# Optimization experiments

Hardware: AMD Instinct MI355X
Metric: run time of the kernel (lower is better)

Reference implementation:

```python
import jax, jax.numpy as jnp
import numpy as np

B, N, M, BUCKETS = 4096, 2048, 2048, 16
T = 100.0  # softmax temperature from module (self.T = 100)


def _make_values(buckets):
    b = buckets // 2
    v = np.zeros((buckets, 1), np.float32)
    for i in range(buckets):
        v[i, 0] = 1.0 / 2.0 ** (b - i) if i < b else -1.0 / 2.0 ** (i - b)
    return jnp.asarray(v)


def setup_inputs() -> dict:
    key = jax.random.key(0)
    ks = jax.random.split(key, 7)
    scale = 1.0 / np.sqrt(M)  # nn.Linear default init range
    return {
        "x": jax.random.normal(ks[0], (B, M), jnp.float32),
        "x_hash": jax.random.normal(ks[1], (B, M), jnp.float32),
        "weight": jax.random.uniform(ks[2], (N, M), jnp.float32, -scale, scale),
        "bias": jax.random.uniform(ks[3], (N,), jnp.float32, -scale, scale),
        "a0": jax.random.normal(ks[4], (BUCKETS, 1), jnp.float32),
        "a1": jax.random.normal(ks[5], (BUCKETS, 1), jnp.float32),
        "a2": jax.random.normal(ks[6], (BUCKETS, 1), jnp.float32),
        "values": _make_values(BUCKETS),
    }


def reference(x, x_hash, weight, bias, a0, a1, a2, values):
    n, m = weight.shape
    fcw = weight.reshape(1, -1)                       # [1, N*M]
    # rank-1 outer products + bias: fx [buckets, N*M]
    fx = a1 @ fcw + a2 @ (fcw * fcw) + a0
    probs = jax.nn.softmax(fx * T, axis=0)            # softmax over buckets
    hash_weight = (probs.T @ values).reshape(n, m)    # [N, M]
    out = x @ weight.T + bias                         # [B, N]
    out_hash = x_hash @ hash_weight.T + bias          # [B, N]
    return out, out_hash
```

## Files before the change

### kernel.cpp

```cpp
#include <hip/hip_runtime.h>
#include <hip/hip_bf16.h>

typedef __attribute__((ext_vector_type(8))) short bf16x8;
typedef __attribute__((ext_vector_type(4))) float f32x4;
typedef __attribute__((ext_vector_type(8))) unsigned short u16x8;
typedef __attribute__((ext_vector_type(4))) unsigned short u16x4;

__device__ __forceinline__ unsigned short f2bf_rtne(float f) {
    unsigned int u = __float_as_uint(f);
    u += 0x7FFFu + ((u >> 16) & 1u);
    return (unsigned short)(u >> 16);
}

__device__ __forceinline__ void gl2lds16(const void* g, void* l) {
    __builtin_amdgcn_global_load_lds((const __attribute__((address_space(1))) void*)g,
                                     (__attribute__((address_space(3))) void*)l, 16, 0, 0);
}

#define NB 16
__global__ void prep_all(const float* __restrict__ x, const float* __restrict__ xh,
                         const float* __restrict__ w,
                         const float* __restrict__ a0, const float* __restrict__ a1,
                         const float* __restrict__ a2, const float* __restrict__ vals,
                         unsigned short* __restrict__ xb, unsigned short* __restrict__ xhb,
                         unsigned short* __restrict__ wbf, unsigned short* __restrict__ hwbf) {
    const int job = blockIdx.y;
    const int stride = gridDim.x * blockDim.x;
    int i = blockIdx.x * blockDim.x + threadIdx.x;
    if (job < 2) {
        const float* in = job ? xh : x;
        unsigned short* out = job ? xhb : xb;
        const int n8 = (4096 * 2048) / 8;
        for (; i < n8; i += stride) {
            const float4* p = (const float4*)in + (size_t)i * 2;
            float4 v0 = p[0];
            float4 v1 = p[1];
            u16x8 r;
            r[0] = f2bf_rtne(v0.x); r[1] = f2bf_rtne(v0.y); r[2] = f2bf_rtne(v0.z); r[3] = f2bf_rtne(v0.w);
            r[4] = f2bf_rtne(v1.x); r[5] = f2bf_rtne(v1.y); r[6] = f2bf_rtne(v1.z); r[7] = f2bf_rtne(v1.w);
            *((u16x8*)out + i) = r;
        }
    } else {
        float A0[NB], A1[NB], A2[NB], V[NB];
#pragma unroll
        for (int b = 0; b < NB; ++b) {
            A0[b] = a0[b] * 100.0f;
            A1[b] = a1[b] * 100.0f;
            A2[b] = a2[b] * 100.0f;
            V[b]  = vals[b];
        }
        const int n4 = (2048 * 2048) / 4;
        for (; i < n4; i += stride) {
            float4 wv = ((const float4*)w)[i];
            float win[4] = {wv.x, wv.y, wv.z, wv.w};
            u16x4 wr, hr;
#pragma unroll
            for (int c = 0; c < 4; ++c) {
                float xx = win[c];
                float x2 = xx * xx;
                float l[NB];
                float mx = -1e30f;
#pragma unroll
                for (int b = 0; b < NB; ++b) {
                    l[b] = fmaf(A1[b], xx, fmaf(A2[b], x2, A0[b]));
                    mx = fmaxf(mx, l[b]);
                }
                float s = 0.0f, acc = 0.0f;
#pragma unroll
                for (int b = 0; b < NB; ++b) {
                    float e = __expf(l[b] - mx);
                    s += e;
                    acc = fmaf(e, V[b], acc);
                }
                wr[c] = f2bf_rtne(xx);
                hr[c] = f2bf_rtne(acc / s);
            }
            *((u16x4*)wbf + i)  = wr;
            *((u16x4*)hwbf + i) = hr;
        }
    }
}

__global__ __launch_bounds__(512, 2) void gemm256(
    const unsigned short* __restrict__ Ax, const unsigned short* __restrict__ Ah,
    const unsigned short* __restrict__ Bw, const unsigned short* __restrict__ Bh,
    const float* __restrict__ bias,
    float* __restrict__ Cx, float* __restrict__ Chh) {
    const int K = 2048, N = 2048;

    __shared__ unsigned short lds[65536];

    const unsigned short* A  = blockIdx.z ? Ah : Ax;
    const unsigned short* Bm = blockIdx.z ? Bh : Bw;
    float* C = blockIdx.z ? Chh : Cx;

    const int tid  = threadIdx.x;
    const int lane = tid & 63;
    const int wid  = tid >> 6;
    const int wr = wid >> 2;
    const int wc = wid & 3;
    const int fr = lane & 15;
    const int fq = lane >> 4;
    const int brow = blockIdx.x;
    const int bcol = blockIdx.y;

    const int srow = tid >> 3;
    const int sg8  = ((tid & 7) ^ (srow & 7)) * 8;
    const unsigned short* gA = A  + (size_t)(brow * 256 + srow) * K + sg8;
    const unsigned short* gB = Bm + (size_t)(bcol * 256 + srow) * K + sg8;
    const int wbase = wid * 512;

    const int g0 = (fq ^ (fr & 7)) * 8;
    const int g1 = g0 ^ 32;

#define STAGE_A(buf, h, j) {                                                    \
    const unsigned short* _g = gA + (size_t)((h) * 128) * K + (j) * 64;         \
    gl2lds16(_g,                  lds + (buf) * 16384 + (h) * 8192 + wbase);    \
    gl2lds16(_g + (size_t)64 * K, lds + (buf) * 16384 + (h) * 8192 + 4096 + wbase); }
#define STAGE_B(buf, h, j) {                                                    \
    const unsigned short* _g = gB + (size_t)((h) * 128) * K + (j) * 64;         \
    gl2lds16(_g,                  lds + 32768 + (buf) * 16384 + (h) * 8192 + wbase); \
    gl2lds16(_g + (size_t)64 * K, lds + 32768 + (buf) * 16384 + (h) * 8192 + 4096 + wbase); }

#define LDA(dst, buf, mblk) {                                                   \
    const unsigned short* _p = lds + (buf) * 16384 + (wr * 128 + (mblk) * 16 + fr) * 64; \
    dst[0] = *(const bf16x8*)(_p + g0);                                         \
    dst[1] = *(const bf16x8*)(_p + g1); }
#define LDB(dst, buf, nblk) {                                                   \
    const unsigned short* _p = lds + 32768 + (buf) * 16384 + (wc * 64 + (nblk) * 16 + fr) * 64; \
    dst[0] = *(const bf16x8*)(_p + g0);                                         \
    dst[1] = *(const bf16x8*)(_p + g1); }

#define MM(mi, n, kk, AF) acc[mi][n] = __builtin_amdgcn_mfma_f32_16x16x32_bf16(AF[kk], bfr[n][kk], acc[mi][n], 0, 0, 0)

#define PHASE(q, buf, STG, GATE) {                                              \
    if ((q) == 0) {                                                             \
        LDB(bfr[0], buf, 0); LDB(bfr[1], buf, 1);                               \
        LDB(bfr[2], buf, 2); LDB(bfr[3], buf, 3);                               \
    }                                                                           \
    LDA(af0, buf, 2 * (q)); LDA(af1, buf, 2 * (q) + 1);                         \
    STG;                                                                        \
    __builtin_amdgcn_s_barrier();                                               \
    asm volatile("s_waitcnt lgkmcnt(0)" ::: "memory");                          \
    __builtin_amdgcn_s_setprio(1);                                              \
    MM(2*(q),0,0,af0); MM(2*(q),0,1,af0); MM(2*(q)+1,0,0,af1); MM(2*(q)+1,0,1,af1); \
    MM(2*(q),1,0,af0); MM(2*(q),1,1,af0); MM(2*(q)+1,1,0,af1); MM(2*(q)+1,1,1,af1); \
    MM(2*(q),2,0,af0); MM(2*(q),2,1,af0); MM(2*(q)+1,2,0,af1); MM(2*(q)+1,2,1,af1); \
    MM(2*(q),3,0,af0); MM(2*(q),3,1,af0); MM(2*(q)+1,3,0,af1); MM(2*(q)+1,3,1,af1); \
    __builtin_amdgcn_s_setprio(0);                                              \
    GATE;                                                                       \
    __builtin_amdgcn_s_barrier(); }

    STAGE_A(0, 0, 0); STAGE_A(0, 1, 0);
    STAGE_B(0, 0, 0); STAGE_B(0, 1, 0);
    STAGE_B(1, 0, 1); STAGE_B(1, 1, 1);
    asm volatile("s_waitcnt vmcnt(4)" ::: "memory");
    __builtin_amdgcn_s_barrier();

    f32x4 acc[8][4] = {};
    bf16x8 bfr[4][2], af0[2], af1[2];

#pragma unroll 1
    for (int t = 0; t < 15; ++t) {
        const int j1 = 2 * t + 1, j2 = 2 * t + 2, j3 = 2 * t + 3;
        PHASE(0, 0, STAGE_A(1, 0, j1), );
        PHASE(1, 0, STAGE_A(1, 1, j1), );
        PHASE(2, 0, STAGE_B(0, 0, j2), );
        PHASE(3, 0, STAGE_B(0, 1, j2), asm volatile("s_waitcnt vmcnt(4)" ::: "memory"));
        PHASE(0, 1, STAGE_A(0, 0, j2), );
        PHASE(1, 1, STAGE_A(0, 1, j2), );
        PHASE(2, 1, STAGE_B(1, 0, j3), );
        PHASE(3, 1, STAGE_B(1, 1, j3), asm volatile("s_waitcnt vmcnt(4)" ::: "memory"));
    }
    PHASE(0, 0, STAGE_A(1, 0, 31), );
    PHASE(1, 0, STAGE_A(1, 1, 31), );
    PHASE(2, 0, , );
    PHASE(3, 0, , asm volatile("s_waitcnt vmcnt(0)" ::: "memory"));
    PHASE(0, 1, , );
    PHASE(1, 1, , );
    PHASE(2, 1, , );
    PHASE(3, 1, , );

#pragma unroll
    for (int n = 0; n < 4; ++n) {
        const int col = bcol * 256 + wc * 64 + n * 16 + fr;
        const float bv = bias[col];
#pragma unroll
        for (int m = 0; m < 8; ++m) {
            const int row0 = brow * 256 + wr * 128 + m * 16 + fq * 4;
#pragma unroll
            for (int r = 0; r < 4; ++r)
                C[(size_t)(row0 + r) * N + col] = acc[m][n][r] + bv;
        }
    }
#undef STAGE_A
#undef STAGE_B
#undef LDA
#undef LDB
#undef MM
#undef PHASE
}

extern "C" void kernel_launch(void* const* d_in, const int* in_sizes, int n_in,
                              void* d_out, int out_size, void* d_ws, size_t ws_size,
                              hipStream_t stream) {
    const float* x    = (const float*)d_in[0];
    const float* xh   = (const float*)d_in[1];
    const float* w    = (const float*)d_in[2];
    const float* bias = (const float*)d_in[3];
    const float* a0   = (const float*)d_in[4];
    const float* a1   = (const float*)d_in[5];
    const float* a2   = (const float*)d_in[6];
    const float* vals = (const float*)d_in[7];

    float* out  = (float*)d_out;
    float* outh = out + (size_t)4096 * 2048;

    char* ws = (char*)d_ws;
    unsigned short* xb  = (unsigned short*)(ws);
    unsigned short* xhb = (unsigned short*)(ws + (size_t)16 * 1024 * 1024);
    unsigned short* wb  = (unsigned short*)(ws + (size_t)32 * 1024 * 1024);
    unsigned short* hwb = (unsigned short*)(ws + (size_t)40 * 1024 * 1024);

    prep_all<<<dim3(1024, 3), 256, 0, stream>>>(x, xh, w, a0, a1, a2, vals, xb, xhb, wb, hwb);

    dim3 grid(4096 / 256, 2048 / 256, 2);
    gemm256<<<grid, 512, 0, stream>>>(xb, xhb, wb, hwb, bias, out, outh);
}
```

Baseline: 102.2 us.

## Switch GEMM inner loop to 32x32x16 bf16 MFMA tiles

Replaces the 16x16x32 MFMA tiling with 32x32x16 MFMA instructions. Each wave now computes a 4x2 grid of 32x32 accumulators, and the LDS fragment loads and the epilogue row mapping are reworked to match the new lane layout. Larger MFMA tiles raise arithmetic per LDS read and cut the instruction count per phase. The risk is a different LDS bank access pattern and longer MFMA dependency latency. The prep kernel grid is also doubled in x, which changes how that preprocessing work is split across blocks.

```diff
diff --git a/kernel.cpp b/kernel.cpp
--- a/kernel.cpp
+++ b/kernel.cpp
@@ -2,7 +2,7 @@
 #include <hip/hip_bf16.h>
 
 typedef __attribute__((ext_vector_type(8))) short bf16x8;
-typedef __attribute__((ext_vector_type(4))) float f32x4;
+typedef __attribute__((ext_vector_type(16))) float f32x16;
 typedef __attribute__((ext_vector_type(8))) unsigned short u16x8;
 typedef __attribute__((ext_vector_type(4))) unsigned short u16x4;
 
@@ -99,8 +99,8 @@
     const int wid  = tid >> 6;
     const int wr = wid >> 2;
     const int wc = wid & 3;
-    const int fr = lane & 15;
-    const int fq = lane >> 4;
+    const int l31 = lane & 31;
+    const int kh  = lane >> 5;
     const int brow = blockIdx.x;
     const int bcol = blockIdx.y;
 
@@ -110,8 +110,11 @@
     const unsigned short* gB = Bm + (size_t)(bcol * 256 + srow) * K + sg8;
     const int wbase = wid * 512;
 
-    const int g0 = (fq ^ (fr & 7)) * 8;
-    const int g1 = g0 ^ 32;
+    const int ax = lane & 7;
+    const int gq[4] = { ((0 + kh) ^ ax) * 8, ((2 + kh) ^ ax) * 8,
+                        ((4 + kh) ^ ax) * 8, ((6 + kh) ^ ax) * 8 };
+    const int aBase = (wr * 128 + l31) * 64;
+    const int bBase = 32768 + (wc * 64 + l31) * 64;
 
 #define STAGE_A(buf, h, j) {                                                    \
     const unsigned short* _g = gA + (size_t)((h) * 128) * K + (j) * 64;         \
@@ -122,31 +125,33 @@
     gl2lds16(_g,                  lds + 32768 + (buf) * 16384 + (h) * 8192 + wbase); \
     gl2lds16(_g + (size_t)64 * K, lds + 32768 + (buf) * 16384 + (h) * 8192 + 4096 + wbase); }
 
-#define LDA(dst, buf, mblk) {                                                   \
-    const unsigned short* _p = lds + (buf) * 16384 + (wr * 128 + (mblk) * 16 + fr) * 64; \
-    dst[0] = *(const bf16x8*)(_p + g0);                                         \
-    dst[1] = *(const bf16x8*)(_p + g1); }
-#define LDB(dst, buf, nblk) {                                                   \
-    const unsigned short* _p = lds + 32768 + (buf) * 16384 + (wc * 64 + (nblk) * 16 + fr) * 64; \
-    dst[0] = *(const bf16x8*)(_p + g0);                                         \
-    dst[1] = *(const bf16x8*)(_p + g1); }
-
-#define MM(mi, n, kk, AF) acc[mi][n] = __builtin_amdgcn_mfma_f32_16x16x32_bf16(AF[kk], bfr[n][kk], acc[mi][n], 0, 0, 0)
+#define MM(m, n, q) acc[m][n] = __builtin_amdgcn_mfma_f32_32x32x16_bf16(af[m], bq[n][q], acc[m][n], 0, 0, 0)
 
 #define PHASE(q, buf, STG, GATE) {                                              \
-    if ((q) == 0) {                                                             \
-        LDB(bfr[0], buf, 0); LDB(bfr[1], buf, 1);                               \
-        LDB(bfr[2], buf, 2); LDB(bfr[3], buf, 3);                               \
+    if ((q) == 0) {                     \
+        const unsigned short* _pb = lds + (buf) * 16384 + bBase;                \
+        bq[0][0] = *(const bf16x8*)(_pb + gq[0]);                               \
+        bq[0][1] = *(const bf16x8*)(_pb + gq[1]);                               \
+        bq[0][2] = *(const bf16x8*)(_pb + gq[2]);                               \
+        bq[0][3] = *(const bf16x8*)(_pb + gq[3]);                               \
+        bq[1][0] = *(const bf16x8*)(_pb + 2048 + gq[0]);                        \
+        bq[1][1] = *(const bf16x8*)(_pb + 2048 + gq[1]);                        \
+        bq[1][2] = *(const bf16x8*)(_pb + 2048 + gq[2]);                        \
+        bq[1][3] = *(const bf16x8*)(_pb + 2048 + gq[3]);                        \
     }                                                                           \
-    LDA(af0, buf, 2 * (q)); LDA(af1, buf, 2 * (q) + 1);                         \
+    {                                                                           \
+        const unsigned short* _pa = lds + (buf) * 16384 + aBase + gq[q];        \
+        af[0] = *(const bf16x8*)(_pa);                                          \
+        af[1] = *(const bf16x8*)(_pa + 2048);                                   \
+        af[2] = *(const bf16x8*)(_pa + 4096);                                   \
+        af[3] = *(const bf16x8*)(_pa + 6144);                                   \
+    }                                                                           \
     STG;                                                                        \
     __builtin_amdgcn_s_barrier();                                               \
     asm volatile("s_waitcnt lgkmcnt(0)" ::: "memory");                          \
     __builtin_amdgcn_s_setprio(1);                                              \
-    MM(2*(q),0,0,af0); MM(2*(q),0,1,af0); MM(2*(q)+1,0,0,af1); MM(2*(q)+1,0,1,af1); \
-    MM(2*(q),1,0,af0); MM(2*(q),1,1,af0); MM(2*(q)+1,1,0,af1); MM(2*(q)+1,1,1,af1); \
-    MM(2*(q),2,0,af0); MM(2*(q),2,1,af0); MM(2*(q)+1,2,0,af1); MM(2*(q)+1,2,1,af1); \
-    MM(2*(q),3,0,af0); MM(2*(q),3,1,af0); MM(2*(q)+1,3,0,af1); MM(2*(q)+1,3,1,af1); \
+    MM(0, 0, q); MM(1, 0, q); MM(2, 0, q); MM(3, 0, q);                         \
+    MM(0, 1, q); MM(1, 1, q); MM(2, 1, q); MM(3, 1, q);                         \
     __builtin_amdgcn_s_setprio(0);                                              \
     GATE;                                                                       \
     __builtin_amdgcn_s_barrier(); }
@@ -157,8 +162,8 @@
     asm volatile("s_waitcnt vmcnt(4)" ::: "memory");
     __builtin_amdgcn_s_barrier();
 
-    f32x4 acc[8][4] = {};
-    bf16x8 bfr[4][2], af0[2], af1[2];
+    f32x16 acc[4][2] = {};
+    bf16x8 af[4], bq[2][4];
 
 #pragma unroll 1
     for (int t = 0; t < 15; ++t) {
@@ -182,21 +187,21 @@
     PHASE(3, 1, , );
 
 #pragma unroll
-    for (int n = 0; n < 4; ++n) {
-        const int col = bcol * 256 + wc * 64 + n * 16 + fr;
+    for (int n = 0; n < 2; ++n) {
+        const int col = bcol * 256 + wc * 64 + n * 32 + l31;
         const float bv = bias[col];
 #pragma unroll
-        for (int m = 0; m < 8; ++m) {
-            const int row0 = brow * 256 + wr * 128 + m * 16 + fq * 4;
-#pragma unroll
-            for (int r = 0; r < 4; ++r)
-                C[(size_t)(row0 + r) * N + col] = acc[m][n][r] + bv;
+        for (int m = 0; m < 4; ++m) {
+            const int row_base = brow * 256 + wr * 128 + m * 32 + 4 * kh;
+#pragma unroll
+            for (int r = 0; r < 16; ++r) {
+                const int row = row_base + (r & 3) + 8 * (r >> 2);
+                C[(size_t)row * N + col] = acc[m][n][r] + bv;
+            }
         }
     }
 #undef STAGE_A
 #undef STAGE_B
-#undef LDA
-#undef LDB
 #undef MM
 #undef PHASE
 }
@@ -222,7 +227,7 @@
     unsigned short* wb  = (unsigned short*)(ws + (size_t)32 * 1024 * 1024);
     unsigned short* hwb = (unsigned short*)(ws + (size_t)40 * 1024 * 1024);
 
-    prep_all<<<dim3(1024, 3), 256, 0, stream>>>(x, xh, w, a0, a1, a2, vals, xb, xhb, wb, hwb);
+    prep_all<<<dim3(2048, 3), 256, 0, stream>>>(x, xh, w, a0, a1, a2, vals, xb, xhb, wb, hwb);
 
     dim3 grid(4096 / 256, 2048 / 256, 2);
     gemm256<<<grid, 512, 0, stream>>>(xb, xhb, wb, hwb, bias, out, outh);
```

New measurement: 108.2 us. +5.9%, slower.

## Double-buffer A fragments in registers and read LDS one phase ahead

Applied to the files above, without the earlier changes.

The GEMM main loop now keeps two sets of A-fragment registers. LDS reads for the next phase are issued right after the barrier, while the current phase's MFMAs run on fragments loaded earlier, instead of waiting on lgkmcnt(0) before every MFMA block. The explicit waitcnt and the barrier before compute are dropped, so the compiler is left to insert waits. The prep kernel's grid is also doubled in x. This uses more VGPRs, and the prep launch only stays correct if prep_all handles the larger grid through bounds checks or a stride loop.

```diff
diff --git a/kernel.cpp b/kernel.cpp
--- a/kernel.cpp
+++ b/kernel.cpp
@@ -122,33 +122,32 @@
     gl2lds16(_g,                  lds + 32768 + (buf) * 16384 + (h) * 8192 + wbase); \
     gl2lds16(_g + (size_t)64 * K, lds + 32768 + (buf) * 16384 + (h) * 8192 + 4096 + wbase); }
 
-#define LDA(dst, buf, mblk) {                                                   \
+#define RDA(dst, buf, mblk) {                                                   \
     const unsigned short* _p = lds + (buf) * 16384 + (wr * 128 + (mblk) * 16 + fr) * 64; \
     dst[0] = *(const bf16x8*)(_p + g0);                                         \
     dst[1] = *(const bf16x8*)(_p + g1); }
-#define LDB(dst, buf, nblk) {                                                   \
+#define RDB(dst, buf, nblk) {                                                   \
     const unsigned short* _p = lds + 32768 + (buf) * 16384 + (wc * 64 + (nblk) * 16 + fr) * 64; \
     dst[0] = *(const bf16x8*)(_p + g0);                                         \
     dst[1] = *(const bf16x8*)(_p + g1); }
+#define RD_BURST(buf) { RDB(bfr[0], buf, 0); RDB(bfr[1], buf, 1);               \
+                        RDB(bfr[2], buf, 2); RDB(bfr[3], buf, 3); }
 
 #define MM(mi, n, kk, AF) acc[mi][n] = __builtin_amdgcn_mfma_f32_16x16x32_bf16(AF[kk], bfr[n][kk], acc[mi][n], 0, 0, 0)
 
-#define PHASE(q, buf, STG, GATE) {                                              \
-    if ((q) == 0) {                                                             \
-        LDB(bfr[0], buf, 0); LDB(bfr[1], buf, 1);                               \
-        LDB(bfr[2], buf, 2); LDB(bfr[3], buf, 3);                               \
-    }                                                                           \
-    LDA(af0, buf, 2 * (q)); LDA(af1, buf, 2 * (q) + 1);                         \
+#define PH(q, A0_, A1_, RDS, STG, GATE) {                                       \
+    __builtin_amdgcn_s_barrier();                                               \
+    asm volatile("" ::: "memory");                                              \
+    RDS;                                                                        \
     STG;                                                                        \
-    __builtin_amdgcn_s_barrier();                                               \
-    asm volatile("s_waitcnt lgkmcnt(0)" ::: "memory");                          \
     __builtin_amdgcn_s_setprio(1);                                              \
-    MM(2*(q),0,0,af0); MM(2*(q),0,1,af0); MM(2*(q)+1,0,0,af1); MM(2*(q)+1,0,1,af1); \
-    MM(2*(q),1,0,af0); MM(2*(q),1,1,af0); MM(2*(q)+1,1,0,af1); MM(2*(q)+1,1,1,af1); \
-    MM(2*(q),2,0,af0); MM(2*(q),2,1,af0); MM(2*(q)+1,2,0,af1); MM(2*(q)+1,2,1,af1); \
-    MM(2*(q),3,0,af0); MM(2*(q),3,1,af0); MM(2*(q)+1,3,0,af1); MM(2*(q)+1,3,1,af1); \
+    MM(2*(q),0,0,A0_); MM(2*(q),0,1,A0_); MM(2*(q)+1,0,0,A1_); MM(2*(q)+1,0,1,A1_); \
+    MM(2*(q),1,0,A0_); MM(2*(q),1,1,A0_); MM(2*(q)+1,1,0,A1_); MM(2*(q)+1,1,1,A1_); \
+    MM(2*(q),2,0,A0_); MM(2*(q),2,1,A0_); MM(2*(q)+1,2,0,A1_); MM(2*(q)+1,2,1,A1_); \
+    MM(2*(q),3,0,A0_); MM(2*(q),3,1,A0_); MM(2*(q)+1,3,0,A1_); MM(2*(q)+1,3,1,A1_); \
     __builtin_amdgcn_s_setprio(0);                                              \
     GATE;                                                                       \
+    asm volatile("" ::: "memory");                                              \
     __builtin_amdgcn_s_barrier(); }
 
     STAGE_A(0, 0, 0); STAGE_A(0, 1, 0);
@@ -158,28 +157,31 @@
     __builtin_amdgcn_s_barrier();
 
     f32x4 acc[8][4] = {};
-    bf16x8 bfr[4][2], af0[2], af1[2];
+    bf16x8 bfr[4][2], aU0[2], aU1[2], aV0[2], aV1[2];
 
 #pragma unroll 1
     for (int t = 0; t < 15; ++t) {
         const int j1 = 2 * t + 1, j2 = 2 * t + 2, j3 = 2 * t + 3;
-        PHASE(0, 0, STAGE_A(1, 0, j1), );
-        PHASE(1, 0, STAGE_A(1, 1, j1), );
-        PHASE(2, 0, STAGE_B(0, 0, j2), );
-        PHASE(3, 0, STAGE_B(0, 1, j2), asm volatile("s_waitcnt vmcnt(4)" ::: "memory"));
-        PHASE(0, 1, STAGE_A(0, 0, j2), );
-        PHASE(1, 1, STAGE_A(0, 1, j2), );
-        PHASE(2, 1, STAGE_B(1, 0, j3), );
-        PHASE(3, 1, STAGE_B(1, 1, j3), asm volatile("s_waitcnt vmcnt(4)" ::: "memory"));
+        PH(0, aU0, aU1, { RD_BURST(0); RDA(aU0,0,0); RDA(aU1,0,1); RDA(aV0,0,2); RDA(aV1,0,3); },
+           STAGE_A(1, 0, j1), );
+        PH(1, aV0, aV1, { RDA(aU0,0,4); RDA(aU1,0,5); }, STAGE_A(1, 1, j1), );
+        PH(2, aU0, aU1, { RDA(aV0,0,6); RDA(aV1,0,7); }, STAGE_B(0, 0, j2), );
+        PH(3, aV0, aV1, , STAGE_B(0, 1, j2), asm volatile("s_waitcnt vmcnt(4)" ::: "memory"));
+        PH(0, aU0, aU1, { RD_BURST(1); RDA(aU0,1,0); RDA(aU1,1,1); RDA(aV0,1,2); RDA(aV1,1,3); },
+           STAGE_A(0, 0, j2), );
+        PH(1, aV0, aV1, { RDA(aU0,1,4); RDA(aU1,1,5); }, STAGE_A(0, 1, j2), );
+        PH(2, aU0, aU1, { RDA(aV0,1,6); RDA(aV1,1,7); }, STAGE_B(1, 0, j3), );
+        PH(3, aV0, aV1, , STAGE_B(1, 1, j3), asm volatile("s_waitcnt vmcnt(4)" ::: "memory"));
     }
-    PHASE(0, 0, STAGE_A(1, 0, 31), );
-    PHASE(1, 0, STAGE_A(1, 1, 31), );
-    PHASE(2, 0, , );
-    PHASE(3, 0, , asm volatile("s_waitcnt vmcnt(0)" ::: "memory"));
-    PHASE(0, 1, , );
-    PHASE(1, 1, , );
-    PHASE(2, 1, , );
-    PHASE(3, 1, , );
+    PH(0, aU0, aU1, { RD_BURST(0); RDA(aU0,0,0); RDA(aU1,0,1); RDA(aV0,0,2); RDA(aV1,0,3); },
+       STAGE_A(1, 0, 31), );
+    PH(1, aV0, aV1, { RDA(aU0,0,4); RDA(aU1,0,5); }, STAGE_A(1, 1, 31), );
+    PH(2, aU0, aU1, { RDA(aV0,0,6); RDA(aV1,0,7); }, , );
+    PH(3, aV0, aV1, , , asm volatile("s_waitcnt vmcnt(0)" ::: "memory"));
+    PH(0, aU0, aU1, { RD_BURST(1); RDA(aU0,1,0); RDA(aU1,1,1); RDA(aV0,1,2); RDA(aV1,1,3); }, , );
+    PH(1, aV0, aV1, { RDA(aU0,1,4); RDA(aU1,1,5); }, , );
+    PH(2, aU0, aU1, { RDA(aV0,1,6); RDA(aV1,1,7); }, , );
+    PH(3, aV0, aV1, , , );
 
 #pragma unroll
     for (int n = 0; n < 4; ++n) {
@@ -195,10 +197,11 @@
     }
 #undef STAGE_A
 #undef STAGE_B
-#undef LDA
-#undef LDB
+#undef RDA
+#undef RDB
+#undef RD_BURST
 #undef MM
-#undef PHASE
+#undef PH
 }
 
 extern "C" void kernel_launch(void* const* d_in, const int* in_sizes, int n_in,
@@ -222,7 +225,7 @@
     unsigned short* wb  = (unsigned short*)(ws + (size_t)32 * 1024 * 1024);
     unsigned short* hwb = (unsigned short*)(ws + (size_t)40 * 1024 * 1024);
 
-    prep_all<<<dim3(1024, 3), 256, 0, stream>>>(x, xh, w, a0, a1, a2, vals, xb, xhb, wb, hwb);
+    prep_all<<<dim3(2048, 3), 256, 0, stream>>>(x, xh, w, a0, a1, a2, vals, xb, xhb, wb, hwb);
 
     dim3 grid(4096 / 256, 2048 / 256, 2);
     gemm256<<<grid, 512, 0, stream>>>(xb, xhb, wb, hwb, bias, out, outh);
```

Result: faster. 98.81 us (-3.3%).
